# Kernel tuning notes

Hardware: AMD Instinct MI355X
Metric: run time of the kernel (lower is better)

The kernel has to match this reference:

```python
import jax, jax.numpy as jnp
import numpy as np


def setup_inputs() -> dict:
    key = jax.random.key(0)
    k1, k2, k3, k4 = jax.random.split(key, 4)
    B, A, N = 16, 4096, 128
    positions = jax.random.normal(k1, (B, A, 3), dtype=jnp.float32)
    neighbors = jax.random.randint(k2, (B, A, N), 0, A, dtype=jnp.int64)
    cell = jax.random.normal(k3, (B, 3, 3), dtype=jnp.float32)
    cell_offsets = jax.random.normal(k4, (B, A, N, 3), dtype=jnp.float32)
    neighbor_mask = jax.random.bernoulli(jax.random.fold_in(key, 5), 0.9, (B, A, N))
    return {
        "positions": positions,
        "neighbors": neighbors,
        "cell": cell,
        "cell_offsets": cell_offsets,
        "neighbor_mask": neighbor_mask,
    }


def reference(positions, neighbors, cell, cell_offsets, neighbor_mask):
    B, A, N = neighbors.shape
    # gather neighbor positions: (B, A, N, 3)
    flat_idx = neighbors.reshape(B, A * N)
    pos_xyz = jnp.take_along_axis(positions, flat_idx[:, :, None], axis=1).reshape(B, A, N, 3)
    dist_vec = pos_xyz - positions[:, :, None, :]
    # periodic cell offsets: (B, A*N, 3) @ (B, 3, 3) -> (B, A, N, 3)
    offsets = jnp.einsum("band,bde->bane", cell_offsets, cell)
    dist_vec = dist_vec + offsets
    distances = jnp.sqrt(jnp.sum(dist_vec * dist_vec, axis=-1))  # (B, A, N)
    distances = jnp.where(neighbor_mask, distances, 0.0)
    return distances
```

## Files before the change

### kernel.cpp

```cpp
#include <hip/hip_runtime.h>


#define A_DIM 4096
#define N_DIM 128

__global__ __launch_bounds__(256) void atom_distances_kernel(
    const float* __restrict__ positions,
    const int*   __restrict__ neighbors,
    const float* __restrict__ cell,
    const float* __restrict__ cell_offsets,
    const int*   __restrict__ mask,
    float* __restrict__ out)
{
    const int ELEMS_PER_BLOCK = 1024;
    const int BLOCKS_PER_BATCH = (A_DIM * N_DIM) / ELEMS_PER_BLOCK;

    const int b = blockIdx.x / BLOCKS_PER_BATCH;
    const int r = (blockIdx.x % BLOCKS_PER_BATCH) * ELEMS_PER_BLOCK + threadIdx.x * 4;
    const int a = r >> 7;
    const int e = b * (A_DIM * N_DIM) + r;

    const float* cb = cell + b * 9;
    const float c00 = cb[0], c01 = cb[1], c02 = cb[2];
    const float c10 = cb[3], c11 = cb[4], c12 = cb[5];
    const float c20 = cb[6], c21 = cb[7], c22 = cb[8];

    const float* pb = positions + b * (A_DIM * 3);
    const float ax = pb[a * 3 + 0];
    const float ay = pb[a * 3 + 1];
    const float az = pb[a * 3 + 2];

    const int4 nb = *(const int4*)(neighbors + e);
    const int4 mk = *(const int4*)(mask + e);
    const float4* co = (const float4*)(cell_offsets + (size_t)e * 3);
    const float4 o0 = co[0];
    const float4 o1 = co[1];
    const float4 o2 = co[2];

    float cox[4], coy[4], coz[4];
    cox[0] = o0.x; coy[0] = o0.y; coz[0] = o0.z;
    cox[1] = o0.w; coy[1] = o1.x; coz[1] = o1.y;
    cox[2] = o1.z; coy[2] = o1.w; coz[2] = o2.x;
    cox[3] = o2.y; coy[3] = o2.z; coz[3] = o2.w;

    const int jj[4] = { nb.x, nb.y, nb.z, nb.w };
    const int mm[4] = { mk.x, mk.y, mk.z, mk.w };

    float res[4];
#pragma unroll
    for (int k = 0; k < 4; ++k) {
        const float* pj = pb + jj[k] * 3;
        const float px = pj[0];
        const float py = pj[1];
        const float pz = pj[2];
        const float dx = px - ax + cox[k] * c00 + coy[k] * c10 + coz[k] * c20;
        const float dy = py - ay + cox[k] * c01 + coy[k] * c11 + coz[k] * c21;
        const float dz = pz - az + cox[k] * c02 + coy[k] * c12 + coz[k] * c22;
        const float d = sqrtf(dx * dx + dy * dy + dz * dz);
        res[k] = mm[k] ? d : 0.0f;
    }

    *(float4*)(out + e) = make_float4(res[0], res[1], res[2], res[3]);
}

extern "C" void kernel_launch(void* const* d_in, const int* in_sizes, int n_in,
                              void* d_out, int out_size, void* d_ws, size_t ws_size,
                              hipStream_t stream) {
    const float* positions    = (const float*)d_in[0];
    const int*   neighbors    = (const int*)d_in[1];
    const float* cell         = (const float*)d_in[2];
    const float* cell_offsets = (const float*)d_in[3];
    const int*   mask         = (const int*)d_in[4];
    float* out = (float*)d_out;

    const int total = out_size;
    const int blocks = total / 1024;
    atom_distances_kernel<<<blocks, 256, 0, stream>>>(
        positions, neighbors, cell, cell_offsets, mask, out);
}
```

Baseline: 230.7 us.

## Stage per-batch positions in LDS and gather neighbors from shared memory

Each block now loads the full batch's atom positions into a 4096-entry float4 LDS array, then processes 32 atoms' neighbor lists with 1024 threads, gathering neighbor positions from LDS instead of global memory. This targets the cost of scattered global gathers of positions. In exchange every block re-reads 48 KB of positions to handle 4096 outputs, adds a barrier, and uses 64 KB LDS which limits occupancy.

After: 211.0 us. -8.6%, faster.

```diff
diff --git a/kernel.cpp b/kernel.cpp
--- a/kernel.cpp
+++ b/kernel.cpp
@@ -3,8 +3,11 @@
 
 #define A_DIM 4096
 #define N_DIM 128
+#define B_DIM 16
+#define ATOMS_PER_BLOCK 32
+#define THREADS 1024
 
-__global__ __launch_bounds__(256) void atom_distances_kernel(
+__global__ __launch_bounds__(THREADS) void atom_distances_lds_kernel(
     const float* __restrict__ positions,
     const int*   __restrict__ neighbors,
     const float* __restrict__ cell,
@@ -12,23 +15,28 @@
     const int*   __restrict__ mask,
     float* __restrict__ out)
 {
-    const int ELEMS_PER_BLOCK = 1024;
-    const int BLOCKS_PER_BATCH = (A_DIM * N_DIM) / ELEMS_PER_BLOCK;
+    __shared__ float4 lpos[A_DIM];
 
-    const int b = blockIdx.x / BLOCKS_PER_BATCH;
-    const int r = (blockIdx.x % BLOCKS_PER_BATCH) * ELEMS_PER_BLOCK + threadIdx.x * 4;
-    const int a = r >> 7;
-    const int e = b * (A_DIM * N_DIM) + r;
+    const int BLOCKS_PER_BATCH = A_DIM / ATOMS_PER_BLOCK;
+    const int b  = blockIdx.x / BLOCKS_PER_BATCH;
+    const int a0 = (blockIdx.x % BLOCKS_PER_BATCH) * ATOMS_PER_BLOCK;
+
+    const float* pb = positions + b * (A_DIM * 3);
+    for (int j = threadIdx.x; j < A_DIM; j += THREADS) {
+        lpos[j] = make_float4(pb[j * 3 + 0], pb[j * 3 + 1], pb[j * 3 + 2], 0.0f);
+    }
+    __syncthreads();
+
+    const int r = threadIdx.x * 4;
+    const int a = a0 + (r >> 7);
+    const int e = (b * A_DIM + a0) * N_DIM + r;
 
     const float* cb = cell + b * 9;
     const float c00 = cb[0], c01 = cb[1], c02 = cb[2];
     const float c10 = cb[3], c11 = cb[4], c12 = cb[5];
     const float c20 = cb[6], c21 = cb[7], c22 = cb[8];
 
-    const float* pb = positions + b * (A_DIM * 3);
-    const float ax = pb[a * 3 + 0];
-    const float ay = pb[a * 3 + 1];
-    const float az = pb[a * 3 + 2];
+    const float4 ap = lpos[a];
 
     const int4 nb = *(const int4*)(neighbors + e);
     const int4 mk = *(const int4*)(mask + e);
@@ -46,16 +54,16 @@
     const int jj[4] = { nb.x, nb.y, nb.z, nb.w };
     const int mm[4] = { mk.x, mk.y, mk.z, mk.w };
 
+    float4 pj[4];
+#pragma unroll
+    for (int k = 0; k < 4; ++k) pj[k] = lpos[jj[k]];
+
     float res[4];
 #pragma unroll
     for (int k = 0; k < 4; ++k) {
-        const float* pj = pb + jj[k] * 3;
-        const float px = pj[0];
-        const float py = pj[1];
-        const float pz = pj[2];
-        const float dx = px - ax + cox[k] * c00 + coy[k] * c10 + coz[k] * c20;
-        const float dy = py - ay + cox[k] * c01 + coy[k] * c11 + coz[k] * c21;
-        const float dz = pz - az + cox[k] * c02 + coy[k] * c12 + coz[k] * c22;
+        const float dx = pj[k].x - ap.x + cox[k] * c00 + coy[k] * c10 + coz[k] * c20;
+        const float dy = pj[k].y - ap.y + cox[k] * c01 + coy[k] * c11 + coz[k] * c21;
+        const float dz = pj[k].z - ap.z + cox[k] * c02 + coy[k] * c12 + coz[k] * c22;
         const float d = sqrtf(dx * dx + dy * dy + dz * dz);
         res[k] = mm[k] ? d : 0.0f;
     }
@@ -73,8 +81,7 @@
     const int*   mask         = (const int*)d_in[4];
     float* out = (float*)d_out;
 
-    const int total = out_size;
-    const int blocks = total / 1024;
-    atom_distances_kernel<<<blocks, 256, 0, stream>>>(
+    const int blocks = B_DIM * (A_DIM / ATOMS_PER_BLOCK);
+    atom_distances_lds_kernel<<<blocks, THREADS, 0, stream>>>(
         positions, neighbors, cell, cell_offsets, mask, out);
 }
```
